# Kernel tuning notes

Hardware: AMD Instinct MI355X
Metric: run time of the kernel (lower is better)

## Reference

```python
import jax, jax.numpy as jnp
import numpy as np

EMBED_DIM = 1024
NUM_HEADS = 16
HEAD_DIM = EMBED_DIM // NUM_HEADS
SCALE = HEAD_DIM ** -0.5
B, S = 2, 2048


def setup_inputs() -> dict:
    key = jax.random.key(0)
    ks = jax.random.split(key, 10)
    def lin(kw, kb, fan_in):
        bound = 1.0 / np.sqrt(fan_in)
        W = jax.random.uniform(kw, (EMBED_DIM, EMBED_DIM), jnp.float32, -bound, bound)
        b = jax.random.uniform(kb, (EMBED_DIM,), jnp.float32, -bound, bound)
        return W, b
    Wq, bq = lin(ks[0], ks[1], EMBED_DIM)
    Wk, bk = lin(ks[2], ks[3], EMBED_DIM)
    Wv, bv = lin(ks[4], ks[5], EMBED_DIM)
    Wo, bo = lin(ks[6], ks[7], EMBED_DIM)
    x = jax.random.normal(ks[8], (B, S, EMBED_DIM), jnp.float32)
    # sparsity_mask: True where token kept (rand > sparsity with sparsity=0.5)
    sparsity_mask = jax.random.randint(ks[9], (B, NUM_HEADS, S), 0, 2).astype(bool)
    return {"x": x, "sparsity_mask": sparsity_mask,
            "Wq": Wq, "bq": bq, "Wk": Wk, "bk": bk,
            "Wv": Wv, "bv": bv, "Wo": Wo, "bo": bo}


def reference(x, sparsity_mask, Wq, bq, Wk, bk, Wv, bv, Wo, bo):
    b, s, _ = x.shape
    def heads(W, bias):
        # torch Linear: x @ W.T + b ; then [b, s, h, d] -> [b, h, s, d]
        y = x @ W.T + bias
        return y.reshape(b, s, NUM_HEADS, HEAD_DIM).transpose(0, 2, 1, 3)
    q = heads(Wq, bq)
    k = heads(Wk, bk)
    v = heads(Wv, bv)
    m = sparsity_mask[..., None].astype(q.dtype)  # [b, h, s, 1]
    q = q * m
    k = k * m
    attn = jnp.einsum('bhqd,bhkd->bhqk', q, k) * SCALE
    attn = jax.nn.softmax(attn, axis=-1)
    out = jnp.einsum('bhqk,bhkd->bhqd', attn, v)
    out = out.transpose(0, 2, 1, 3).reshape(b, s, EMBED_DIM)
    return out @ Wo.T + bo
```

## Files before the change

### kernel.cpp

```cpp
#include <hip/hip_runtime.h>

#define DEV __device__ __forceinline__

typedef __bf16 bf16x8 __attribute__((ext_vector_type(8)));
typedef __bf16 bf16x4 __attribute__((ext_vector_type(4)));
typedef float f32x4 __attribute__((ext_vector_type(4)));
typedef unsigned u32x4 __attribute__((ext_vector_type(4)));
typedef unsigned short ushort_t;

static constexpr int EMBED = 1024;
static constexpr int NHEAD = 16;
static constexpr int HDIM  = 64;
static constexpr int S_    = 2048;
static constexpr float SCALE_L2E = 0.125f * 1.44269504088896340736f;

DEV ushort_t f2bf(float f) {
  unsigned u = __builtin_bit_cast(unsigned, f);
  unsigned r = (u + 0x7fffu + ((u >> 16) & 1u)) >> 16;
  return (ushort_t)r;
}

#define GLOAD_LDS16(g, l)                                                   \
  __builtin_amdgcn_global_load_lds(                                         \
      (const __attribute__((address_space(1))) unsigned int*)(g),           \
      (__attribute__((address_space(3))) unsigned int*)(l), 16, 0, 0)

#define DRAIN_VM() asm volatile("s_waitcnt vmcnt(0)" ::: "memory")

__global__ __launch_bounds__(256) void convert_kernel(
    const float* __restrict__ x,
    const float* __restrict__ wq, const float* __restrict__ wk,
    const float* __restrict__ wv, const float* __restrict__ wo,
    ushort_t* __restrict__ xb, ushort_t* __restrict__ wqb,
    ushort_t* __restrict__ wkb, ushort_t* __restrict__ wvb,
    ushort_t* __restrict__ wob) {
  size_t i = ((size_t)blockIdx.x * blockDim.x + threadIdx.x) * 4;
  const float* src; ushort_t* dst; size_t off;
  if (i < 4194304u)      { src = x;  dst = xb;  off = i; }
  else if (i < 5242880u) { src = wq; dst = wqb; off = i - 4194304u; }
  else if (i < 6291456u) { src = wk; dst = wkb; off = i - 5242880u; }
  else if (i < 7340032u) { src = wv; dst = wvb; off = i - 6291456u; }
  else                   { src = wo; dst = wob; off = i - 7340032u; }
  float4 v = *(const float4*)(src + off);
  ushort4 o;
  o.x = f2bf(v.x); o.y = f2bf(v.y); o.z = f2bf(v.z); o.w = f2bf(v.w);
  *(ushort4*)(dst + off) = o;
}

__global__ __launch_bounds__(256) void qkv_kernel(
    const ushort_t* __restrict__ xb, const ushort_t* __restrict__ wqb,
    const ushort_t* __restrict__ wkb, const ushort_t* __restrict__ wvb,
    const float* __restrict__ bq, const float* __restrict__ bk,
    const float* __restrict__ bv, const int* __restrict__ mask,
    ushort_t* __restrict__ qo, ushort_t* __restrict__ ko,
    ushort_t* __restrict__ vto) {
  __shared__ __align__(16) unsigned char ldsA[16384];
  __shared__ __align__(16) unsigned char ldsB[16384];
  __shared__ float maskf[2][128];

  const int bid  = blockIdx.x;
  const int tid  = threadIdx.x;
  const int lane = tid & 63;
  const int w    = tid >> 6;
  const int wm   = (w >> 1) * 64;
  const int wn   = (w & 1) * 64;
  const int rl   = lane & 15;
  const int kg   = lane >> 4;

  int mode, ar0, br0;
  const ushort_t *A, *Bm;
  const float* bias;
  if (bid < 512) {
    mode = bid >> 8;
    int t = bid & 255;
    ar0 = (t & 31) * 128;
    br0 = (t >> 5) * 128;
    A = xb; Bm = mode ? wkb : wqb; bias = mode ? bk : bq;
  } else {
    mode = 2;
    int t = bid - 512;
    ar0 = (t & 7) * 128;
    br0 = (t >> 3) * 128;
    A = wvb; Bm = xb; bias = bv;
  }

  if (mode < 2) {
    int hl = tid >> 7, sl = tid & 127;
    int m = ar0 + sl;
    int b = m >> 11, s = m & 2047;
    int h = (br0 >> 6) + hl;
    maskf[hl][sl] = (float)mask[((size_t)b * NHEAD + h) * S_ + s];
  }

  f32x4 acc[4][4];
#pragma unroll
  for (int i = 0; i < 4; ++i)
#pragma unroll
    for (int j = 0; j < 4; ++j) acc[i][j] = f32x4{0.f, 0.f, 0.f, 0.f};

  auto STAGE = [&](int kt) {
    const int k0 = kt * 64;
#pragma unroll
    for (int s = 0; s < 8; ++s) {
      const int basev = s * 256 + w * 64;
      const int Lb = basev & 1023;
      const int L = Lb + lane;
      const int row = L >> 3;
      const int gu = (L & 7) ^ (row & 7);
      if (s < 4) {
        GLOAD_LDS16(A + (size_t)(ar0 + row) * EMBED + k0 + gu * 8, &ldsA[Lb * 16]);
      } else {
        GLOAD_LDS16(Bm + (size_t)(br0 + row) * EMBED + k0 + gu * 8, &ldsB[Lb * 16]);
      }
    }
  };

  for (int kt = 0; kt < 16; ++kt) {
    if (kt) __syncthreads();
    STAGE(kt);
    DRAIN_VM();
    __syncthreads();
#pragma unroll
    for (int kk = 0; kk < 2; ++kk) {
      bf16x8 af[4], bfr[4];
#pragma unroll
      for (int mb = 0; mb < 4; ++mb) {
        const int row = wm + mb * 16 + rl;
        const int off = (kk * 64 + kg * 16) ^ ((row & 7) << 4);
        af[mb] = *(const bf16x8*)(ldsA + row * 128 + off);
      }
#pragma unroll
      for (int nb = 0; nb < 4; ++nb) {
        const int row = wn + nb * 16 + rl;
        const int off = (kk * 64 + kg * 16) ^ ((row & 7) << 4);
        bfr[nb] = *(const bf16x8*)(ldsB + row * 128 + off);
      }
#pragma unroll
      for (int mb = 0; mb < 4; ++mb)
#pragma unroll
        for (int nb = 0; nb < 4; ++nb)
          acc[mb][nb] = __builtin_amdgcn_mfma_f32_16x16x32_bf16(
              af[mb], bfr[nb], acc[mb][nb], 0, 0, 0);
    }
  }

#pragma unroll
  for (int mb = 0; mb < 4; ++mb)
#pragma unroll
    for (int nb = 0; nb < 4; ++nb)
#pragma unroll
      for (int r = 0; r < 4; ++r) {
        int row_l = wm + mb * 16 + kg * 4 + r;
        int col_l = wn + nb * 16 + rl;
        float v = acc[mb][nb][r];
        if (mode < 2) {
          int m = ar0 + row_l, n = br0 + col_l;
          v = (v + bias[n]) * maskf[col_l >> 6][row_l];
          if (mode == 0) v *= SCALE_L2E;
          int b = m >> 11, s = m & 2047, h = n >> 6, d = n & 63;
          ushort_t* o = mode ? ko : qo;
          o[(((size_t)(b * NHEAD + h)) * S_ + s) * HDIM + d] = f2bf(v);
        } else {
          int n = ar0 + row_l, m = br0 + col_l;
          v += bias[n];
          int b = m >> 11, s = m & 2047, h = n >> 6, d = n & 63;
          vto[(((size_t)(b * NHEAD + h)) * HDIM + d) * S_ + s] = f2bf(v);
        }
      }
}

__global__ __launch_bounds__(256) void gemm_o_kernel(
    const ushort_t* __restrict__ A, const ushort_t* __restrict__ Bm,
    const float* __restrict__ bias, float* __restrict__ outp) {
  __shared__ __align__(16) unsigned char ldsA[16384];
  __shared__ __align__(16) unsigned char ldsB[16384];

  const int tid  = threadIdx.x;
  const int lane = tid & 63;
  const int w    = tid >> 6;
  const int ar0  = blockIdx.x * 128;
  const int br0  = blockIdx.y * 128;
  const int wm   = (w >> 1) * 64;
  const int wn   = (w & 1) * 64;
  const int rl   = lane & 15;
  const int kg   = lane >> 4;

  f32x4 acc[4][4];
#pragma unroll
  for (int i = 0; i < 4; ++i)
#pragma unroll
    for (int j = 0; j < 4; ++j) acc[i][j] = f32x4{0.f, 0.f, 0.f, 0.f};

  auto STAGE = [&](int kt) {
    const int k0 = kt * 64;
#pragma unroll
    for (int s = 0; s < 8; ++s) {
      const int basev = s * 256 + w * 64;
      const int Lb = basev & 1023;
      const int L = Lb + lane;
      const int row = L >> 3;
      const int gu = (L & 7) ^ (row & 7);
      if (s < 4) {
        GLOAD_LDS16(A + (size_t)(ar0 + row) * EMBED + k0 + gu * 8, &ldsA[Lb * 16]);
      } else {
        GLOAD_LDS16(Bm + (size_t)(br0 + row) * EMBED + k0 + gu * 8, &ldsB[Lb * 16]);
      }
    }
  };

  for (int kt = 0; kt < 16; ++kt) {
    if (kt) __syncthreads();
    STAGE(kt);
    DRAIN_VM();
    __syncthreads();
#pragma unroll
    for (int kk = 0; kk < 2; ++kk) {
      bf16x8 af[4], bfr[4];
#pragma unroll
      for (int mb = 0; mb < 4; ++mb) {
        const int row = wm + mb * 16 + rl;
        const int off = (kk * 64 + kg * 16) ^ ((row & 7) << 4);
        af[mb] = *(const bf16x8*)(ldsA + row * 128 + off);
      }
#pragma unroll
      for (int nb = 0; nb < 4; ++nb) {
        const int row = wn + nb * 16 + rl;
        const int off = (kk * 64 + kg * 16) ^ ((row & 7) << 4);
        bfr[nb] = *(const bf16x8*)(ldsB + row * 128 + off);
      }
#pragma unroll
      for (int mb = 0; mb < 4; ++mb)
#pragma unroll
        for (int nb = 0; nb < 4; ++nb)
          acc[mb][nb] = __builtin_amdgcn_mfma_f32_16x16x32_bf16(
              af[mb], bfr[nb], acc[mb][nb], 0, 0, 0);
    }
  }

#pragma unroll
  for (int mb = 0; mb < 4; ++mb)
#pragma unroll
    for (int nb = 0; nb < 4; ++nb)
#pragma unroll
      for (int r = 0; r < 4; ++r) {
        int m = ar0 + wm + mb * 16 + kg * 4 + r;
        int n = br0 + wn + nb * 16 + rl;
        outp[(size_t)m * EMBED + n] = acc[mb][nb][r] + bias[n];
      }
}

__global__ __launch_bounds__(128) void attn_kernel(
    const ushort_t* __restrict__ qp, const ushort_t* __restrict__ kp,
    const ushort_t* __restrict__ vtp, ushort_t* __restrict__ ao) {
  __shared__ __align__(16) unsigned char ldsK[2][8192];
  __shared__ __align__(16) unsigned char ldsV[2][8192];
  __shared__ __align__(16) unsigned char ldsP[2][4096];

  const int tid  = threadIdx.x;
  const int lane = tid & 63;
  const int w    = tid >> 6;
  const int bh   = blockIdx.x;
  const int q0   = blockIdx.y * 64 + w * 32;
  const int rl   = lane & 15;
  const int kg   = lane >> 4;
  const int pswz = (rl & 7) << 4;

  const bf16x8 ones = __builtin_bit_cast(bf16x8,
      u32x4{0x3F803F80u, 0x3F803F80u, 0x3F803F80u, 0x3F803F80u});

  bf16x8 qa[2][2];
#pragma unroll
  for (int qb = 0; qb < 2; ++qb)
#pragma unroll
    for (int kk = 0; kk < 2; ++kk)
      qa[qb][kk] = *(const bf16x8*)(qp + ((size_t)bh * S_ + q0 + qb * 16 + rl) * HDIM +
                                    kk * 32 + kg * 8);

  f32x4 o_acc[2][4];
  f32x4 o_l[2];
#pragma unroll
  for (int qb = 0; qb < 2; ++qb) {
#pragma unroll
    for (int nb = 0; nb < 4; ++nb) o_acc[qb][nb] = f32x4{0.f, 0.f, 0.f, 0.f};
    o_l[qb] = f32x4{0.f, 0.f, 0.f, 0.f};
  }

  unsigned char* pb = ldsP[w];

  auto STAGE = [&](int kt, int bsel) {
#pragma unroll
    for (int s = 0; s < 8; ++s) {
      const int Lb = (s & 3) * 128 + w * 64;
      const int L = Lb + lane;
      const int row = L >> 3;
      const int gu = (L & 7) ^ (row & 7);
      if (s < 4) {
        GLOAD_LDS16(kp + ((size_t)bh * S_ + (size_t)kt * 64 + row) * HDIM + gu * 8,
                    &ldsK[bsel][Lb * 16]);
      } else {
        GLOAD_LDS16(vtp + ((size_t)bh * HDIM + row) * S_ + (size_t)kt * 64 + gu * 8,
                    &ldsV[bsel][Lb * 16]);
      }
    }
  };

  STAGE(0, 0);
  DRAIN_VM();
  __syncthreads();
  int cb = 0;
  for (int kt = 0; kt < 32; ++kt) {
    if (kt < 31) STAGE(kt + 1, cb ^ 1);

    f32x4 sa[2][4];
#pragma unroll
    for (int qb = 0; qb < 2; ++qb)
#pragma unroll
      for (int nb = 0; nb < 4; ++nb) sa[qb][nb] = f32x4{0.f, 0.f, 0.f, 0.f};
#pragma unroll
    for (int nb = 0; nb < 4; ++nb) {
      const int row = nb * 16 + rl;
#pragma unroll
      for (int kk = 0; kk < 2; ++kk) {
        bf16x8 kf = *(const bf16x8*)(ldsK[cb] + row * 128 +
                                     ((kk * 64 + kg * 16) ^ ((row & 7) << 4)));
        sa[0][nb] = __builtin_amdgcn_mfma_f32_16x16x32_bf16(kf, qa[0][kk], sa[0][nb], 0, 0, 0);
        sa[1][nb] = __builtin_amdgcn_mfma_f32_16x16x32_bf16(kf, qa[1][kk], sa[1][nb], 0, 0, 0);
      }
    }

#pragma unroll
    for (int qb = 0; qb < 2; ++qb)
#pragma unroll
      for (int nb = 0; nb < 4; ++nb) {
        bf16x4 pk4;
#pragma unroll
        for (int r = 0; r < 4; ++r)
          pk4[r] = (__bf16)__builtin_amdgcn_exp2f(sa[qb][nb][r]);
        *(bf16x4*)(pb + (qb * 16 + rl) * 128 + ((nb * 32 + kg * 8) ^ pswz)) = pk4;
      }
    asm volatile("s_waitcnt lgkmcnt(0)" ::: "memory");
    __builtin_amdgcn_sched_barrier(0);

    bf16x8 pa[2][2];
#pragma unroll
    for (int qb = 0; qb < 2; ++qb)
#pragma unroll
      for (int kk = 0; kk < 2; ++kk)
        pa[qb][kk] = *(const bf16x8*)(pb + (qb * 16 + rl) * 128 +
                                      ((kk * 64 + kg * 16) ^ pswz));

    o_l[0] = __builtin_amdgcn_mfma_f32_16x16x32_bf16(pa[0][0], ones, o_l[0], 0, 0, 0);
    o_l[0] = __builtin_amdgcn_mfma_f32_16x16x32_bf16(pa[0][1], ones, o_l[0], 0, 0, 0);
    o_l[1] = __builtin_amdgcn_mfma_f32_16x16x32_bf16(pa[1][0], ones, o_l[1], 0, 0, 0);
    o_l[1] = __builtin_amdgcn_mfma_f32_16x16x32_bf16(pa[1][1], ones, o_l[1], 0, 0, 0);

#pragma unroll
    for (int nb = 0; nb < 4; ++nb) {
      const int row = nb * 16 + rl;
#pragma unroll
      for (int kk = 0; kk < 2; ++kk) {
        bf16x8 vb = *(const bf16x8*)(ldsV[cb] + row * 128 +
                                     ((kk * 64 + kg * 16) ^ ((row & 7) << 4)));
        o_acc[0][nb] = __builtin_amdgcn_mfma_f32_16x16x32_bf16(pa[0][kk], vb, o_acc[0][nb], 0, 0, 0);
        o_acc[1][nb] = __builtin_amdgcn_mfma_f32_16x16x32_bf16(pa[1][kk], vb, o_acc[1][nb], 0, 0, 0);
      }
    }

    DRAIN_VM();
    __syncthreads();
    cb ^= 1;
  }

  const int b = bh >> 4, h = bh & 15;
#pragma unroll
  for (int qb = 0; qb < 2; ++qb)
#pragma unroll
    for (int r = 0; r < 4; ++r) {
      float linv = 1.0f / o_l[qb][r];
      const int row = q0 + qb * 16 + kg * 4 + r;
#pragma unroll
      for (int nb = 0; nb < 4; ++nb) {
        float v = o_acc[qb][nb][r] * linv;
        ao[((size_t)b * S_ + row) * EMBED + h * HDIM + nb * 16 + rl] = f2bf(v);
      }
    }
}

extern "C" void kernel_launch(void* const* d_in, const int* in_sizes, int n_in,
                              void* d_out, int out_size, void* d_ws, size_t ws_size,
                              hipStream_t stream) {
  const float* x    = (const float*)d_in[0];
  const int*   mask = (const int*)d_in[1];
  const float* Wq   = (const float*)d_in[2];
  const float* bq   = (const float*)d_in[3];
  const float* Wk   = (const float*)d_in[4];
  const float* bk   = (const float*)d_in[5];
  const float* Wv   = (const float*)d_in[6];
  const float* bv   = (const float*)d_in[7];
  const float* Wo   = (const float*)d_in[8];
  const float* bo   = (const float*)d_in[9];

  char* ws = (char*)d_ws;
  ushort_t* xb  = (ushort_t*)(ws);
  ushort_t* wqb = (ushort_t*)(ws + 8388608);
  ushort_t* wkb = (ushort_t*)(ws + 10485760);
  ushort_t* wvb = (ushort_t*)(ws + 12582912);
  ushort_t* wob = (ushort_t*)(ws + 14680064);
  ushort_t* qb  = (ushort_t*)(ws + 16777216);
  ushort_t* kb  = (ushort_t*)(ws + 25165824);
  ushort_t* vtb = (ushort_t*)(ws + 33554432);
  ushort_t* aob = (ushort_t*)(ws + 41943040);

  hipLaunchKernelGGL(convert_kernel, dim3(8192), dim3(256), 0, stream,
                     x, Wq, Wk, Wv, Wo, xb, wqb, wkb, wvb, wob);
  hipLaunchKernelGGL(qkv_kernel, dim3(768), dim3(256), 0, stream,
                     xb, wqb, wkb, wvb, bq, bk, bv, mask, qb, kb, vtb);
  hipLaunchKernelGGL(attn_kernel, dim3(32, 32), dim3(128), 0, stream,
                     qb, kb, vtb, aob);
  hipLaunchKernelGGL(gemm_o_kernel, dim3(32, 8), dim3(256), 0, stream,
                     aob, wob, bo, (float*)d_out);
}
```

Baseline: 126.4 us.

## Load K and V fragments directly from global into registers, dropping LDS staging

The attention kernel stops staging K and V tiles through double-buffered shared memory via global_load_lds and instead has each wave load its MFMA fragments straight from global memory into registers. The next K tile is prefetched into registers while V is loaded per iteration. This removes the per-iteration block barrier and VM drain and cuts LDS use, and launch_bounds now requests 2 blocks per CU. In exchange, both waves of a block fetch the same K/V data redundantly from global/L2, and register pressure rises from the prefetch buffers.

```diff
diff --git a/kernel.cpp b/kernel.cpp
--- a/kernel.cpp
+++ b/kernel.cpp
@@ -249,11 +249,9 @@
       }
 }
 
-__global__ __launch_bounds__(128) void attn_kernel(
+__global__ __launch_bounds__(128, 2) void attn_kernel(
     const ushort_t* __restrict__ qp, const ushort_t* __restrict__ kp,
     const ushort_t* __restrict__ vtp, ushort_t* __restrict__ ao) {
-  __shared__ __align__(16) unsigned char ldsK[2][8192];
-  __shared__ __align__(16) unsigned char ldsV[2][8192];
   __shared__ __align__(16) unsigned char ldsP[2][4096];
 
   const int tid  = threadIdx.x;
@@ -286,30 +284,34 @@
   }
 
   unsigned char* pb = ldsP[w];
-
-  auto STAGE = [&](int kt, int bsel) {
-#pragma unroll
-    for (int s = 0; s < 8; ++s) {
-      const int Lb = (s & 3) * 128 + w * 64;
-      const int L = Lb + lane;
-      const int row = L >> 3;
-      const int gu = (L & 7) ^ (row & 7);
-      if (s < 4) {
-        GLOAD_LDS16(kp + ((size_t)bh * S_ + (size_t)kt * 64 + row) * HDIM + gu * 8,
-                    &ldsK[bsel][Lb * 16]);
-      } else {
-        GLOAD_LDS16(vtp + ((size_t)bh * HDIM + row) * S_ + (size_t)kt * 64 + gu * 8,
-                    &ldsV[bsel][Lb * 16]);
-      }
-    }
-  };
-
-  STAGE(0, 0);
-  DRAIN_VM();
-  __syncthreads();
-  int cb = 0;
+  const ushort_t* kbp = kp + (size_t)bh * S_ * HDIM;
+  const ushort_t* vbp = vtp + (size_t)bh * HDIM * S_;
+
+  bf16x8 kf[4][2];
+#pragma unroll
+  for (int nb = 0; nb < 4; ++nb)
+#pragma unroll
+    for (int kk = 0; kk < 2; ++kk)
+      kf[nb][kk] = *(const bf16x8*)(kbp + (size_t)(nb * 16 + rl) * HDIM +
+                                    kk * 32 + kg * 8);
+
   for (int kt = 0; kt < 32; ++kt) {
-    if (kt < 31) STAGE(kt + 1, cb ^ 1);
+    bf16x8 vf[4][2];
+#pragma unroll
+    for (int nb = 0; nb < 4; ++nb)
+#pragma unroll
+      for (int kk = 0; kk < 2; ++kk)
+        vf[nb][kk] = *(const bf16x8*)(vbp + (size_t)(nb * 16 + rl) * S_ +
+                                      kt * 64 + kk * 32 + kg * 8);
+    bf16x8 kn[4][2];
+    if (kt < 31) {
+#pragma unroll
+      for (int nb = 0; nb < 4; ++nb)
+#pragma unroll
+        for (int kk = 0; kk < 2; ++kk)
+          kn[nb][kk] = *(const bf16x8*)(kbp + (size_t)((kt + 1) * 64 + nb * 16 + rl) * HDIM +
+                                        kk * 32 + kg * 8);
+    }
 
     f32x4 sa[2][4];
 #pragma unroll
@@ -317,16 +319,12 @@
 #pragma unroll
       for (int nb = 0; nb < 4; ++nb) sa[qb][nb] = f32x4{0.f, 0.f, 0.f, 0.f};
 #pragma unroll
-    for (int nb = 0; nb < 4; ++nb) {
-      const int row = nb * 16 + rl;
+    for (int nb = 0; nb < 4; ++nb)
 #pragma unroll
       for (int kk = 0; kk < 2; ++kk) {
-        bf16x8 kf = *(const bf16x8*)(ldsK[cb] + row * 128 +
-                                     ((kk * 64 + kg * 16) ^ ((row & 7) << 4)));
-        sa[0][nb] = __builtin_amdgcn_mfma_f32_16x16x32_bf16(kf, qa[0][kk], sa[0][nb], 0, 0, 0);
-        sa[1][nb] = __builtin_amdgcn_mfma_f32_16x16x32_bf16(kf, qa[1][kk], sa[1][nb], 0, 0, 0);
-      }
-    }
+        sa[0][nb] = __builtin_amdgcn_mfma_f32_16x16x32_bf16(kf[nb][kk], qa[0][kk], sa[0][nb], 0, 0, 0);
+        sa[1][nb] = __builtin_amdgcn_mfma_f32_16x16x32_bf16(kf[nb][kk], qa[1][kk], sa[1][nb], 0, 0, 0);
+      }
 
 #pragma unroll
     for (int qb = 0; qb < 2; ++qb)
@@ -355,20 +353,19 @@
     o_l[1] = __builtin_amdgcn_mfma_f32_16x16x32_bf16(pa[1][1], ones, o_l[1], 0, 0, 0);
 
 #pragma unroll
-    for (int nb = 0; nb < 4; ++nb) {
-      const int row = nb * 16 + rl;
+    for (int nb = 0; nb < 4; ++nb)
 #pragma unroll
       for (int kk = 0; kk < 2; ++kk) {
-        bf16x8 vb = *(const bf16x8*)(ldsV[cb] + row * 128 +
-                                     ((kk * 64 + kg * 16) ^ ((row & 7) << 4)));
-        o_acc[0][nb] = __builtin_amdgcn_mfma_f32_16x16x32_bf16(pa[0][kk], vb, o_acc[0][nb], 0, 0, 0);
-        o_acc[1][nb] = __builtin_amdgcn_mfma_f32_16x16x32_bf16(pa[1][kk], vb, o_acc[1][nb], 0, 0, 0);
-      }
-    }
-
-    DRAIN_VM();
-    __syncthreads();
-    cb ^= 1;
+        o_acc[0][nb] = __builtin_amdgcn_mfma_f32_16x16x32_bf16(pa[0][kk], vf[nb][kk], o_acc[0][nb], 0, 0, 0);
+        o_acc[1][nb] = __builtin_amdgcn_mfma_f32_16x16x32_bf16(pa[1][kk], vf[nb][kk], o_acc[1][nb], 0, 0, 0);
+      }
+
+    if (kt < 31) {
+#pragma unroll
+      for (int nb = 0; nb < 4; ++nb)
+#pragma unroll
+        for (int kk = 0; kk < 2; ++kk) kf[nb][kk] = kn[nb][kk];
+    }
   }
 
   const int b = bh >> 4, h = bh & 15;
```

New measurement: 186.2 us. 47.3% more time.
